# Optimization experiments

Measured on AMD Instinct MI355X. Metric: run time of the kernel, lower is better.

The kernel has to match this reference:

```python
import jax, jax.numpy as jnp
import numpy as np

UNITS = 128
FILTERS = 32
KSIZE = 31
B, T, DV, DQ = 64, 1000, 512, 1024


def setup_inputs() -> dict:
    key = jax.random.key(0)
    ks = jax.random.split(key, 12)
    scale = 0.05
    inp = {
        "query": jax.random.normal(ks[0], (B, DQ), jnp.float32),
        "values": jax.random.normal(ks[1], (B, T, DV), jnp.float32),
        "previous_attention_weights": jax.random.uniform(ks[2], (B, T, 1), jnp.float32),
        # learned params
        "Wq": jax.random.normal(ks[3], (DQ, UNITS), jnp.float32) * scale,
        "bq": jnp.zeros((UNITS,), jnp.float32),
        "Wm": jax.random.normal(ks[4], (DV, UNITS), jnp.float32) * scale,
        "bm": jnp.zeros((UNITS,), jnp.float32),
        "Wv": jax.random.normal(ks[5], (UNITS, 1), jnp.float32) * scale,
        "bv": jnp.zeros((1,), jnp.float32),
        "Wconv": jax.random.normal(ks[6], (KSIZE, 1, FILTERS), jnp.float32) * scale,  # [W, Cin, Cout]
        "Wl": jax.random.normal(ks[7], (FILTERS, UNITS), jnp.float32) * scale,
    }
    return inp


def _forward(query, values, prev_w, Wq, bq, Wm, bm, Wv, bv, Wconv, Wl):
    # location features: Conv1D (same padding, no bias) then Dense(tanh, no bias)
    loc = jax.lax.conv_general_dilated(
        prev_w, Wconv, window_strides=(1,), padding="SAME",
        dimension_numbers=("NWC", "WIO", "NWC"))          # [B, T, FILTERS]
    loc = jnp.tanh(loc @ Wl)                                # [B, T, UNITS]
    q = query @ Wq + bq                                     # [B, UNITS]
    m = values @ Wm + bm                                    # [B, T, UNITS]
    score = jnp.tanh(m + q[:, None, :] + loc) @ Wv + bv     # [B, T, 1]
    attention_weights = jax.nn.softmax(score, axis=1)       # softmax over time
    context = jnp.sum(attention_weights * values, axis=1)   # [B, DV]
    return context, attention_weights


def reference(query, values, previous_attention_weights, Wq, bq, Wm, bm, Wv, bv, Wconv, Wl):
    return _forward(query, values, previous_attention_weights,
                    Wq, bq, Wm, bm, Wv, bv, Wconv, Wl)
```

## Files before the change

### kernel.cpp

```cpp
#include <hip/hip_runtime.h>

#define B_  64
#define T_  1000
#define DV_ 512
#define DQ_ 1024
#define U_  128
#define F_  32
#define KS_ 31
#define P_  16
#define CT_ 63

typedef __attribute__((ext_vector_type(8))) short short8;
typedef __attribute__((ext_vector_type(4))) float f32x4;

__device__ __forceinline__ unsigned pk2(float a, float b) {
    union { float f; unsigned u; } x, y;
    x.f = a; y.f = b;
    unsigned ra = (x.u + 0x7FFFu + ((x.u >> 16) & 1u)) >> 16;
    unsigned rb = (y.u + 0x7FFFu + ((y.u >> 16) & 1u)) >> 16;
    return (ra & 0xFFFFu) | (rb << 16);
}

__device__ __forceinline__ float fast_tanh(float x) {
    return 1.0f - 2.0f / (__expf(2.0f * x) + 1.0f);
}

__device__ __forceinline__ short8 pk8(float4 f0, float4 f1) {
    int4 q;
    q.x = pk2(f0.x, f0.y); q.y = pk2(f0.z, f0.w);
    q.z = pk2(f1.x, f1.y); q.w = pk2(f1.z, f1.w);
    return *(short8*)&q;
}

__global__ __launch_bounds__(1024) void prep_qb_kernel(
    const float* __restrict__ Wm, const float* __restrict__ Wl,
    const float* __restrict__ query, const float* __restrict__ Wq,
    const float* __restrict__ bq, const float* __restrict__ bm,
    short* __restrict__ WmX, short* __restrict__ WlX, float* __restrict__ qb)
{
    __shared__ float sh[DQ_ + 8 * U_];
    int blk = blockIdx.x, tid = threadIdx.x;
    if (blk < 9) {
        int g = blk * 1024 + tid;
        if (g < 8192) {
            int kc = g >> 9, e = g & 511;
            int n = e >> 2, q = e & 3;
            int kb = kc * 32 + q * 8;
            int4 p;
            p.x = pk2(Wm[(kb + 0) * U_ + n], Wm[(kb + 1) * U_ + n]);
            p.y = pk2(Wm[(kb + 2) * U_ + n], Wm[(kb + 3) * U_ + n]);
            p.z = pk2(Wm[(kb + 4) * U_ + n], Wm[(kb + 5) * U_ + n]);
            p.w = pk2(Wm[(kb + 6) * U_ + n], Wm[(kb + 7) * U_ + n]);
            ((int4*)WmX)[g] = p;
        } else if (g < 8704) {
            int e = g - 8192;
            int n = e >> 2, q = e & 3;
            int kb = q * 8;
            int4 p;
            p.x = pk2(Wl[(kb + 0) * U_ + n], Wl[(kb + 1) * U_ + n]);
            p.y = pk2(Wl[(kb + 2) * U_ + n], Wl[(kb + 3) * U_ + n]);
            p.z = pk2(Wl[(kb + 4) * U_ + n], Wl[(kb + 5) * U_ + n]);
            p.w = pk2(Wl[(kb + 6) * U_ + n], Wl[(kb + 7) * U_ + n]);
            ((int4*)WlX)[e] = p;
        }
    } else {
        float* qs = sh;
        float* red = sh + DQ_;
        int b = blk - 9;
        qs[tid] = query[b * DQ_ + tid];
        __syncthreads();
        int u = tid & 127, p = tid >> 7;
        float a = 0.f;
        const float* wp = Wq + (size_t)p * 128 * U_ + u;
        const float* qp = qs + p * 128;
#pragma unroll 8
        for (int k = 0; k < 128; ++k) a += qp[k] * wp[(size_t)k * U_];
        red[p * U_ + u] = a;
        __syncthreads();
        if (tid < U_) {
            float s = bq[tid] + bm[tid];
#pragma unroll
            for (int pp = 0; pp < 8; ++pp) s += red[pp * U_ + tid];
            qb[b * U_ + tid] = s;
        }
    }
}

__global__ __launch_bounds__(256) void score_kernel(
    const float* __restrict__ values, const float* __restrict__ prev,
    const float* __restrict__ Wc, const float* __restrict__ Wv,
    const float* __restrict__ bv, const short* __restrict__ WmX,
    const short* __restrict__ WlX, const float* __restrict__ qb,
    float* __restrict__ scores)
{
    __shared__ float WcS[KS_ * F_];
    __shared__ short AsL[128 * 32];
    __shared__ float qbS[2 * U_];
    __shared__ float WvS[U_];

    const int tid = threadIdx.x;
    const int r0 = blockIdx.x * 128;
    const int b0 = r0 / T_;
    const int b1 = (r0 + 127) / T_;

    for (int i = tid; i < KS_ * F_; i += 256) WcS[i] = Wc[i];
    if (tid < U_) WvS[tid] = Wv[tid];
    {
        int bb = (tid < U_) ? b0 : b1;
        qbS[tid] = qb[bb * U_ + (tid & (U_ - 1))];
    }

    const int wv = tid >> 6, lane = tid & 63;
    const int quad = lane >> 4, m15 = lane & 15;
    const int row0 = wv * 32 + m15;
    const float* aP0 = values + (size_t)(r0 + row0) * DV_ + quad * 8;
    const float* aP1 = aP0 + (size_t)16 * DV_;
    const int4* bW  = (const int4*)WmX + m15 * 4 + quad;
    const int4* blW = (const int4*)WlX + m15 * 4 + quad;

    float4 aq0[2][2], aq1[2][2], aq2[2][2];
    int4 bf0[8], bf1[8];
    aq0[0][0] = *(const float4*)(aP0);      aq0[0][1] = *(const float4*)(aP0 + 4);
    aq0[1][0] = *(const float4*)(aP1);      aq0[1][1] = *(const float4*)(aP1 + 4);
    aq1[0][0] = *(const float4*)(aP0 + 32); aq1[0][1] = *(const float4*)(aP0 + 36);
    aq1[1][0] = *(const float4*)(aP1 + 32); aq1[1][1] = *(const float4*)(aP1 + 36);
#pragma unroll
    for (int c = 0; c < 8; ++c) bf0[c] = bW[c * 64];

    __syncthreads();

#pragma unroll
    for (int it = 0; it < 2; ++it) {
        int idx = tid + it * 256;
        int i = idx & 127, fg = idx >> 7;
        int r = r0 + i;
        int b = r / T_;
        int t = r - b * T_;
        const float* pv = prev + b * T_;
        float a8[8] = {};
#pragma unroll
        for (int k = 0; k < KS_; ++k) {
            int tt = t + k - 15;
            float p = ((unsigned)tt < (unsigned)T_) ? pv[tt] : 0.f;
#pragma unroll
            for (int j = 0; j < 8; ++j) a8[j] += p * WcS[k * F_ + fg * 8 + j];
        }
        int4 pq;
        pq.x = pk2(a8[0], a8[1]); pq.y = pk2(a8[2], a8[3]);
        pq.z = pk2(a8[4], a8[5]); pq.w = pk2(a8[6], a8[7]);
        ((int4*)AsL)[i * 4 + (fg ^ ((i >> 1) & 3))] = pq;
    }
    __syncthreads();

    f32x4 acc[2][8] = {};
    {
        int row1 = row0 + 16;
        short8 afl0 = ((const short8*)AsL)[row0 * 4 + (quad ^ ((row0 >> 1) & 3))];
        short8 afl1 = ((const short8*)AsL)[row1 * 4 + (quad ^ ((row1 >> 1) & 3))];
#pragma unroll
        for (int c = 0; c < 8; ++c) {
            int4 bl = blW[c * 64];
            acc[0][c] = __builtin_amdgcn_mfma_f32_16x16x32_bf16(afl0, *(short8*)&bl, acc[0][c], 0, 0, 0);
            acc[1][c] = __builtin_amdgcn_mfma_f32_16x16x32_bf16(afl1, *(short8*)&bl, acc[1][c], 0, 0, 0);
        }
        int qoff[2][4];
#pragma unroll
        for (int g = 0; g < 2; ++g)
#pragma unroll
            for (int v = 0; v < 4; ++v) {
                int r = r0 + wv * 32 + g * 16 + quad * 4 + v;
                qoff[g][v] = ((r / T_) == b0) ? 0 : U_;
            }
#pragma unroll
        for (int g = 0; g < 2; ++g)
#pragma unroll
            for (int c = 0; c < 8; ++c) {
                int col = c * 16 + m15;
#pragma unroll
                for (int v = 0; v < 4; ++v)
                    acc[g][c][v] = qbS[qoff[g][v] + col] + fast_tanh(acc[g][c][v]);
            }
    }

#pragma unroll
    for (int kc = 0; kc < 16; ++kc) {
        if (kc + 2 < 16) {
            aq2[0][0] = *(const float4*)(aP0 + (kc + 2) * 32);
            aq2[0][1] = *(const float4*)(aP0 + (kc + 2) * 32 + 4);
            aq2[1][0] = *(const float4*)(aP1 + (kc + 2) * 32);
            aq2[1][1] = *(const float4*)(aP1 + (kc + 2) * 32 + 4);
        }
        if (kc + 1 < 16) {
#pragma unroll
            for (int c = 0; c < 8; ++c) bf1[c] = bW[(kc + 1) * 512 + c * 64];
        }
        short8 af0 = pk8(aq0[0][0], aq0[0][1]);
        short8 af1 = pk8(aq0[1][0], aq0[1][1]);
#pragma unroll
        for (int c = 0; c < 8; ++c) {
            acc[0][c] = __builtin_amdgcn_mfma_f32_16x16x32_bf16(af0, *(short8*)&bf0[c], acc[0][c], 0, 0, 0);
            acc[1][c] = __builtin_amdgcn_mfma_f32_16x16x32_bf16(af1, *(short8*)&bf0[c], acc[1][c], 0, 0, 0);
        }
#pragma unroll
        for (int g = 0; g < 2; ++g) {
            aq0[g][0] = aq1[g][0]; aq0[g][1] = aq1[g][1];
            aq1[g][0] = aq2[g][0]; aq1[g][1] = aq2[g][1];
        }
#pragma unroll
        for (int c = 0; c < 8; ++c) bf0[c] = bf1[c];
    }

    float psum[2][4] = {};
#pragma unroll
    for (int g = 0; g < 2; ++g)
#pragma unroll
        for (int c = 0; c < 8; ++c) {
            int col = c * 16 + m15;
            float wvv = WvS[col];
#pragma unroll
            for (int v = 0; v < 4; ++v)
                psum[g][v] += fast_tanh(acc[g][c][v]) * wvv;
        }
#pragma unroll
    for (int off = 1; off < 16; off <<= 1) {
#pragma unroll
        for (int g = 0; g < 2; ++g)
#pragma unroll
            for (int v = 0; v < 4; ++v) psum[g][v] += __shfl_xor(psum[g][v], off);
    }
    if (m15 == 0) {
        float bvv = bv[0];
#pragma unroll
        for (int g = 0; g < 2; ++g)
#pragma unroll
            for (int v = 0; v < 4; ++v)
                scores[r0 + wv * 32 + g * 16 + quad * 4 + v] = psum[g][v] + bvv;
    }
}

__global__ void softmax_kernel(const float* __restrict__ s, float* __restrict__ w) {
    __shared__ float red[4];
    int b = blockIdx.x, tid = threadIdx.x;
    const float* sb = s + b * T_;
    float v[4];
    int tv[4];
#pragma unroll
    for (int i = 0; i < 4; ++i) {
        int t = tid + i * 256;
        tv[i] = t;
        v[i] = (t < T_) ? sb[t] : -1e30f;
    }
    float mx = fmaxf(fmaxf(v[0], v[1]), fmaxf(v[2], v[3]));
#pragma unroll
    for (int off = 32; off >= 1; off >>= 1) mx = fmaxf(mx, __shfl_xor(mx, off));
    int wv = tid >> 6, lane = tid & 63;
    if (lane == 0) red[wv] = mx;
    __syncthreads();
    mx = fmaxf(fmaxf(red[0], red[1]), fmaxf(red[2], red[3]));
    float e[4];
    float sum = 0.f;
#pragma unroll
    for (int i = 0; i < 4; ++i) {
        e[i] = (tv[i] < T_) ? __expf(v[i] - mx) : 0.f;
        sum += e[i];
    }
#pragma unroll
    for (int off = 32; off >= 1; off >>= 1) sum += __shfl_xor(sum, off);
    __syncthreads();
    if (lane == 0) red[wv] = sum;
    __syncthreads();
    sum = red[0] + red[1] + red[2] + red[3];
    float inv = 1.0f / sum;
#pragma unroll
    for (int i = 0; i < 4; ++i)
        if (tv[i] < T_) w[b * T_ + tv[i]] = e[i] * inv;
}

__global__ __launch_bounds__(256) void ctx1_kernel(
    const float* __restrict__ values, const float* __restrict__ w,
    float* __restrict__ part)
{
    __shared__ float wS[CT_];
    __shared__ float4 ps[128];
    int b = blockIdx.x, p = blockIdx.y, tid = threadIdx.x;
    int t0 = p * CT_;
    int len = (T_ - t0 < CT_) ? (T_ - t0) : CT_;
    if (tid < len) wS[tid] = w[b * T_ + t0 + tid];
    __syncthreads();
    int cl = tid & 127, tp = tid >> 7;
    const float* vp = values + ((size_t)b * T_ + t0) * DV_ + cl * 4;
    float4 a = {0.f, 0.f, 0.f, 0.f};
#pragma unroll 4
    for (int t = tp; t < len; t += 2) {
        float4 v = *(const float4*)(vp + (size_t)t * DV_);
        float wt = wS[t];
        a.x += wt * v.x; a.y += wt * v.y; a.z += wt * v.z; a.w += wt * v.w;
    }
    if (tp == 1) ps[cl] = a;
    __syncthreads();
    if (tp == 0) {
        float4 o = ps[cl];
        o.x += a.x; o.y += a.y; o.z += a.z; o.w += a.w;
        *(float4*)(part + ((size_t)(b * P_ + p)) * DV_ + cl * 4) = o;
    }
}

__global__ void ctx2_kernel(const float* __restrict__ part, float* __restrict__ ctx) {
    int b = blockIdx.x, tid = threadIdx.x;
    const float* pp = part + (size_t)b * P_ * DV_ + tid * 4;
    float4 s = {0.f, 0.f, 0.f, 0.f};
#pragma unroll
    for (int p = 0; p < P_; ++p) {
        float4 v = *(const float4*)(pp + (size_t)p * DV_);
        s.x += v.x; s.y += v.y; s.z += v.z; s.w += v.w;
    }
    *(float4*)(ctx + (size_t)b * DV_ + tid * 4) = s;
}

extern "C" void kernel_launch(void* const* d_in, const int* in_sizes, int n_in,
                              void* d_out, int out_size, void* d_ws, size_t ws_size,
                              hipStream_t stream) {
    const float* query  = (const float*)d_in[0];
    const float* values = (const float*)d_in[1];
    const float* prev   = (const float*)d_in[2];
    const float* Wq     = (const float*)d_in[3];
    const float* bq     = (const float*)d_in[4];
    const float* Wm     = (const float*)d_in[5];
    const float* bm     = (const float*)d_in[6];
    const float* Wv     = (const float*)d_in[7];
    const float* bv     = (const float*)d_in[8];
    const float* Wc     = (const float*)d_in[9];
    const float* Wl     = (const float*)d_in[10];

    float* out  = (float*)d_out;
    float* ctx  = out;
    float* attw = out + B_ * DV_;

    char* ws = (char*)d_ws;
    float* qb     = (float*)(ws);
    float* scores = (float*)(ws + 32768);
    short* WmX    = (short*)(ws + 288768);
    short* WlX    = (short*)(ws + 419840);
    float* part   = (float*)(ws + 428032);

    prep_qb_kernel<<<73, 1024, 0, stream>>>(Wm, Wl, query, Wq, bq, bm, WmX, WlX, qb);
    score_kernel<<<500, 256, 0, stream>>>(values, prev, Wc, Wv, bv, WmX, WlX, qb, scores);
    softmax_kernel<<<B_, 256, 0, stream>>>(scores, attw);
    ctx1_kernel<<<dim3(B_, P_), 256, 0, stream>>>(values, attw, part);
    ctx2_kernel<<<B_, 128, 0, stream>>>(part, ctx);
}
```

Before: 273.5 us.

## Halve score tile, split query GEMV across blocks, fuse softmax into context kernel

The score kernel now processes 64 rows per block instead of 128, giving 1000 blocks with one 16-row MFMA group per wave and an occupancy hint of 4 blocks per SIMD, which lowers register pressure. The query projection is split into 16 K-slices computed by 64 blocks, and score blocks sum the partials together with the biases. The separate softmax kernel is removed: each context block recomputes the row max and sum from the scores, then writes its own attention weights. This trades a kernel launch and a write-then-read of the weights for redundant softmax reductions in every (batch, chunk) block.

Measured after the change: 348.3 us. 27.3% more time.

```diff
diff --git a/kernel.cpp b/kernel.cpp
--- a/kernel.cpp
+++ b/kernel.cpp
@@ -32,13 +32,12 @@
     return *(short8*)&q;
 }
 
-__global__ __launch_bounds__(1024) void prep_qb_kernel(
+__global__ __launch_bounds__(1024) void prep_kernel(
     const float* __restrict__ Wm, const float* __restrict__ Wl,
     const float* __restrict__ query, const float* __restrict__ Wq,
-    const float* __restrict__ bq, const float* __restrict__ bm,
-    short* __restrict__ WmX, short* __restrict__ WlX, float* __restrict__ qb)
+    short* __restrict__ WmX, short* __restrict__ WlX, float* __restrict__ partQ)
 {
-    __shared__ float sh[DQ_ + 8 * U_];
+    __shared__ float sh[1024];
     int blk = blockIdx.x, tid = threadIdx.x;
     if (blk < 9) {
         int g = blk * 1024 + tid;
@@ -64,75 +63,74 @@
             ((int4*)WlX)[e] = p;
         }
     } else {
-        float* qs = sh;
-        float* red = sh + DQ_;
-        int b = blk - 9;
-        qs[tid] = query[b * DQ_ + tid];
+        int id = blk - 9;
+        int s  = id >> 2;
+        int bg = id & 3;
+        sh[tid] = query[(size_t)(bg * 16 + (tid >> 6)) * DQ_ + s * 64 + (tid & 63)];
         __syncthreads();
-        int u = tid & 127, p = tid >> 7;
-        float a = 0.f;
-        const float* wp = Wq + (size_t)p * 128 * U_ + u;
-        const float* qp = qs + p * 128;
+        int u = tid & 127, h = tid >> 7;
+        const float* wp = Wq + (size_t)(s * 64) * U_ + u;
+        const float* q0 = sh + (h * 2) * 64;
+        const float* q1 = q0 + 64;
+        float a0 = 0.f, a1 = 0.f;
 #pragma unroll 8
-        for (int k = 0; k < 128; ++k) a += qp[k] * wp[(size_t)k * U_];
-        red[p * U_ + u] = a;
-        __syncthreads();
-        if (tid < U_) {
-            float s = bq[tid] + bm[tid];
-#pragma unroll
-            for (int pp = 0; pp < 8; ++pp) s += red[pp * U_ + tid];
-            qb[b * U_ + tid] = s;
-        }
-    }
-}
-
-__global__ __launch_bounds__(256) void score_kernel(
+        for (int k = 0; k < 64; ++k) {
+            float w = wp[(size_t)k * U_];
+            a0 += q0[k] * w; a1 += q1[k] * w;
+        }
+        int b0i = bg * 16 + h * 2;
+        partQ[s * 8192 + b0i * 128 + u]       = a0;
+        partQ[s * 8192 + (b0i + 1) * 128 + u] = a1;
+    }
+}
+
+__global__ __launch_bounds__(256, 4) void score_kernel(
     const float* __restrict__ values, const float* __restrict__ prev,
     const float* __restrict__ Wc, const float* __restrict__ Wv,
     const float* __restrict__ bv, const short* __restrict__ WmX,
-    const short* __restrict__ WlX, const float* __restrict__ qb,
+    const short* __restrict__ WlX, const float* __restrict__ partQ,
+    const float* __restrict__ bq, const float* __restrict__ bm,
     float* __restrict__ scores)
 {
     __shared__ float WcS[KS_ * F_];
-    __shared__ short AsL[128 * 32];
+    __shared__ short AsL[64 * 32];
     __shared__ float qbS[2 * U_];
     __shared__ float WvS[U_];
 
     const int tid = threadIdx.x;
-    const int r0 = blockIdx.x * 128;
+    const int r0 = blockIdx.x * 64;
     const int b0 = r0 / T_;
-    const int b1 = (r0 + 127) / T_;
+    const int b1 = (r0 + 63) / T_;
 
     for (int i = tid; i < KS_ * F_; i += 256) WcS[i] = Wc[i];
     if (tid < U_) WvS[tid] = Wv[tid];
     {
+        int u = tid & (U_ - 1);
         int bb = (tid < U_) ? b0 : b1;
-        qbS[tid] = qb[bb * U_ + (tid & (U_ - 1))];
+        float s = bq[u] + bm[u];
+#pragma unroll
+        for (int sl = 0; sl < 16; ++sl) s += partQ[sl * 8192 + bb * 128 + u];
+        qbS[tid] = s;
     }
 
     const int wv = tid >> 6, lane = tid & 63;
     const int quad = lane >> 4, m15 = lane & 15;
-    const int row0 = wv * 32 + m15;
-    const float* aP0 = values + (size_t)(r0 + row0) * DV_ + quad * 8;
-    const float* aP1 = aP0 + (size_t)16 * DV_;
+    const int row0 = wv * 16 + m15;
+    const float* aP = values + (size_t)(r0 + row0) * DV_ + quad * 8;
     const int4* bW  = (const int4*)WmX + m15 * 4 + quad;
     const int4* blW = (const int4*)WlX + m15 * 4 + quad;
 
-    float4 aq0[2][2], aq1[2][2], aq2[2][2];
-    int4 bf0[8], bf1[8];
-    aq0[0][0] = *(const float4*)(aP0);      aq0[0][1] = *(const float4*)(aP0 + 4);
-    aq0[1][0] = *(const float4*)(aP1);      aq0[1][1] = *(const float4*)(aP1 + 4);
-    aq1[0][0] = *(const float4*)(aP0 + 32); aq1[0][1] = *(const float4*)(aP0 + 36);
-    aq1[1][0] = *(const float4*)(aP1 + 32); aq1[1][1] = *(const float4*)(aP1 + 36);
-#pragma unroll
-    for (int c = 0; c < 8; ++c) bf0[c] = bW[c * 64];
-
-    __syncthreads();
-
-#pragma unroll
-    for (int it = 0; it < 2; ++it) {
-        int idx = tid + it * 256;
-        int i = idx & 127, fg = idx >> 7;
+    float4 aq0[2], aq1[2], aq2[2];
+    int4 bf[8];
+    aq0[0] = *(const float4*)(aP);      aq0[1] = *(const float4*)(aP + 4);
+    aq1[0] = *(const float4*)(aP + 32); aq1[1] = *(const float4*)(aP + 36);
+#pragma unroll
+    for (int c = 0; c < 8; ++c) bf[c] = bW[c * 64];
+
+    __syncthreads();
+
+    {
+        int i = tid & 63, fg = tid >> 6;
         int r = r0 + i;
         int b = r / T_;
         int t = r - b * T_;
@@ -152,96 +150,77 @@
     }
     __syncthreads();
 
-    f32x4 acc[2][8] = {};
+    f32x4 acc[8] = {};
     {
-        int row1 = row0 + 16;
-        short8 afl0 = ((const short8*)AsL)[row0 * 4 + (quad ^ ((row0 >> 1) & 3))];
-        short8 afl1 = ((const short8*)AsL)[row1 * 4 + (quad ^ ((row1 >> 1) & 3))];
+        short8 afl = ((const short8*)AsL)[row0 * 4 + (quad ^ ((row0 >> 1) & 3))];
 #pragma unroll
         for (int c = 0; c < 8; ++c) {
             int4 bl = blW[c * 64];
-            acc[0][c] = __builtin_amdgcn_mfma_f32_16x16x32_bf16(afl0, *(short8*)&bl, acc[0][c], 0, 0, 0);
-            acc[1][c] = __builtin_amdgcn_mfma_f32_16x16x32_bf16(afl1, *(short8*)&bl, acc[1][c], 0, 0, 0);
-        }
-        int qoff[2][4];
-#pragma unroll
-        for (int g = 0; g < 2; ++g)
-#pragma unroll
-            for (int v = 0; v < 4; ++v) {
-                int r = r0 + wv * 32 + g * 16 + quad * 4 + v;
-                qoff[g][v] = ((r / T_) == b0) ? 0 : U_;
-            }
-#pragma unroll
-        for (int g = 0; g < 2; ++g)
-#pragma unroll
-            for (int c = 0; c < 8; ++c) {
-                int col = c * 16 + m15;
-#pragma unroll
-                for (int v = 0; v < 4; ++v)
-                    acc[g][c][v] = qbS[qoff[g][v] + col] + fast_tanh(acc[g][c][v]);
-            }
+            acc[c] = __builtin_amdgcn_mfma_f32_16x16x32_bf16(afl, *(short8*)&bl, acc[c], 0, 0, 0);
+        }
+        int qoff[4];
+#pragma unroll
+        for (int v = 0; v < 4; ++v) {
+            int r = r0 + wv * 16 + quad * 4 + v;
+            qoff[v] = ((r / T_) == b0) ? 0 : U_;
+        }
+#pragma unroll
+        for (int c = 0; c < 8; ++c) {
+            int col = c * 16 + m15;
+#pragma unroll
+            for (int v = 0; v < 4; ++v)
+                acc[c][v] = qbS[qoff[v] + col] + fast_tanh(acc[c][v]);
+        }
     }
 
 #pragma unroll
     for (int kc = 0; kc < 16; ++kc) {
         if (kc + 2 < 16) {
-            aq2[0][0] = *(const float4*)(aP0 + (kc + 2) * 32);
-            aq2[0][1] = *(const float4*)(aP0 + (kc + 2) * 32 + 4);
-            aq2[1][0] = *(const float4*)(aP1 + (kc + 2) * 32);
-            aq2[1][1] = *(const float4*)(aP1 + (kc + 2) * 32 + 4);
-        }
-        if (kc + 1 < 16) {
-#pragma unroll
-            for (int c = 0; c < 8; ++c) bf1[c] = bW[(kc + 1) * 512 + c * 64];
-        }
-        short8 af0 = pk8(aq0[0][0], aq0[0][1]);
-        short8 af1 = pk8(aq0[1][0], aq0[1][1]);
+            aq2[0] = *(const float4*)(aP + (kc + 2) * 32);
+            aq2[1] = *(const float4*)(aP + (kc + 2) * 32 + 4);
+        }
+        short8 af = pk8(aq0[0], aq0[1]);
 #pragma unroll
         for (int c = 0; c < 8; ++c) {
-            acc[0][c] = __builtin_amdgcn_mfma_f32_16x16x32_bf16(af0, *(short8*)&bf0[c], acc[0][c], 0, 0, 0);
-            acc[1][c] = __builtin_amdgcn_mfma_f32_16x16x32_bf16(af1, *(short8*)&bf0[c], acc[1][c], 0, 0, 0);
-        }
-#pragma unroll
-        for (int g = 0; g < 2; ++g) {
-            aq0[g][0] = aq1[g][0]; aq0[g][1] = aq1[g][1];
-            aq1[g][0] = aq2[g][0]; aq1[g][1] = aq2[g][1];
-        }
-#pragma unroll
-        for (int c = 0; c < 8; ++c) bf0[c] = bf1[c];
-    }
-
-    float psum[2][4] = {};
-#pragma unroll
-    for (int g = 0; g < 2; ++g)
-#pragma unroll
-        for (int c = 0; c < 8; ++c) {
-            int col = c * 16 + m15;
-            float wvv = WvS[col];
-#pragma unroll
-            for (int v = 0; v < 4; ++v)
-                psum[g][v] += fast_tanh(acc[g][c][v]) * wvv;
-        }
+            acc[c] = __builtin_amdgcn_mfma_f32_16x16x32_bf16(af, *(short8*)&bf[c], acc[c], 0, 0, 0);
+            if (kc + 1 < 16) bf[c] = bW[(kc + 1) * 512 + c * 64];
+        }
+        aq0[0] = aq1[0]; aq0[1] = aq1[1];
+        aq1[0] = aq2[0]; aq1[1] = aq2[1];
+    }
+
+    float psum[4] = {};
+#pragma unroll
+    for (int c = 0; c < 8; ++c) {
+        int col = c * 16 + m15;
+        float wvv = WvS[col];
+#pragma unroll
+        for (int v = 0; v < 4; ++v)
+            psum[v] += fast_tanh(acc[c][v]) * wvv;
+    }
 #pragma unroll
     for (int off = 1; off < 16; off <<= 1) {
 #pragma unroll
-        for (int g = 0; g < 2; ++g)
-#pragma unroll
-            for (int v = 0; v < 4; ++v) psum[g][v] += __shfl_xor(psum[g][v], off);
+        for (int v = 0; v < 4; ++v) psum[v] += __shfl_xor(psum[v], off);
     }
     if (m15 == 0) {
         float bvv = bv[0];
 #pragma unroll
-        for (int g = 0; g < 2; ++g)
-#pragma unroll
-            for (int v = 0; v < 4; ++v)
-                scores[r0 + wv * 32 + g * 16 + quad * 4 + v] = psum[g][v] + bvv;
-    }
-}
-
-__global__ void softmax_kernel(const float* __restrict__ s, float* __restrict__ w) {
+        for (int v = 0; v < 4; ++v)
+            scores[r0 + wv * 16 + quad * 4 + v] = psum[v] + bvv;
+    }
+}
+
+__global__ __launch_bounds__(256) void ctx1_kernel(
+    const float* __restrict__ values, const float* __restrict__ scores,
+    float* __restrict__ attw, float* __restrict__ part)
+{
+    __shared__ float wS[CT_];
+    __shared__ float4 ps[128];
     __shared__ float red[4];
-    int b = blockIdx.x, tid = threadIdx.x;
-    const float* sb = s + b * T_;
+    int b = blockIdx.x, p = blockIdx.y, tid = threadIdx.x;
+    const float* sb = scores + b * T_;
+
     float v[4];
     int tv[4];
 #pragma unroll
@@ -253,48 +232,38 @@
     float mx = fmaxf(fmaxf(v[0], v[1]), fmaxf(v[2], v[3]));
 #pragma unroll
     for (int off = 32; off >= 1; off >>= 1) mx = fmaxf(mx, __shfl_xor(mx, off));
-    int wv = tid >> 6, lane = tid & 63;
-    if (lane == 0) red[wv] = mx;
+    int wvi = tid >> 6, lane = tid & 63;
+    if (lane == 0) red[wvi] = mx;
     __syncthreads();
     mx = fmaxf(fmaxf(red[0], red[1]), fmaxf(red[2], red[3]));
-    float e[4];
     float sum = 0.f;
 #pragma unroll
-    for (int i = 0; i < 4; ++i) {
-        e[i] = (tv[i] < T_) ? __expf(v[i] - mx) : 0.f;
-        sum += e[i];
-    }
+    for (int i = 0; i < 4; ++i)
+        sum += (tv[i] < T_) ? __expf(v[i] - mx) : 0.f;
 #pragma unroll
     for (int off = 32; off >= 1; off >>= 1) sum += __shfl_xor(sum, off);
     __syncthreads();
-    if (lane == 0) red[wv] = sum;
-    __syncthreads();
-    sum = red[0] + red[1] + red[2] + red[3];
-    float inv = 1.0f / sum;
-#pragma unroll
-    for (int i = 0; i < 4; ++i)
-        if (tv[i] < T_) w[b * T_ + tv[i]] = e[i] * inv;
-}
-
-__global__ __launch_bounds__(256) void ctx1_kernel(
-    const float* __restrict__ values, const float* __restrict__ w,
-    float* __restrict__ part)
-{
-    __shared__ float wS[CT_];
-    __shared__ float4 ps[128];
-    int b = blockIdx.x, p = blockIdx.y, tid = threadIdx.x;
+    if (lane == 0) red[wvi] = sum;
+    __syncthreads();
+    float inv = 1.0f / (red[0] + red[1] + red[2] + red[3]);
+
     int t0 = p * CT_;
     int len = (T_ - t0 < CT_) ? (T_ - t0) : CT_;
-    if (tid < len) wS[tid] = w[b * T_ + t0 + tid];
-    __syncthreads();
+    if (tid < len) {
+        float e = __expf(sb[t0 + tid] - mx) * inv;
+        wS[tid] = e;
+        attw[b * T_ + t0 + tid] = e;
+    }
+    __syncthreads();
+
     int cl = tid & 127, tp = tid >> 7;
     const float* vp = values + ((size_t)b * T_ + t0) * DV_ + cl * 4;
     float4 a = {0.f, 0.f, 0.f, 0.f};
 #pragma unroll 4
     for (int t = tp; t < len; t += 2) {
-        float4 v = *(const float4*)(vp + (size_t)t * DV_);
+        float4 vv = *(const float4*)(vp + (size_t)t * DV_);
         float wt = wS[t];
-        a.x += wt * v.x; a.y += wt * v.y; a.z += wt * v.z; a.w += wt * v.w;
+        a.x += wt * vv.x; a.y += wt * vv.y; a.z += wt * vv.z; a.w += wt * vv.w;
     }
     if (tp == 1) ps[cl] = a;
     __syncthreads();
@@ -337,15 +306,15 @@
     float* attw = out + B_ * DV_;
 
     char* ws = (char*)d_ws;
-    float* qb     = (float*)(ws);
-    float* scores = (float*)(ws + 32768);
-    short* WmX    = (short*)(ws + 288768);
-    short* WlX    = (short*)(ws + 419840);
-    float* part   = (float*)(ws + 428032);
-
-    prep_qb_kernel<<<73, 1024, 0, stream>>>(Wm, Wl, query, Wq, bq, bm, WmX, WlX, qb);
-    score_kernel<<<500, 256, 0, stream>>>(values, prev, Wc, Wv, bv, WmX, WlX, qb, scores);
-    softmax_kernel<<<B_, 256, 0, stream>>>(scores, attw);
-    ctx1_kernel<<<dim3(B_, P_), 256, 0, stream>>>(values, attw, part);
+    float* part   = (float*)(ws);
+    float* partQ  = (float*)(ws);
+    float* scores = (float*)(ws + 2097152);
+    short* WmX    = (short*)(ws + 2097152 + 262144);
+    short* WlX    = (short*)(ws + 2097152 + 262144 + 131072);
+
+    prep_kernel<<<73, 1024, 0, stream>>>(Wm, Wl, query, Wq, WmX, WlX, partQ);
+    score_kernel<<<1000, 256, 0, stream>>>(values, prev, Wc, Wv, bv, WmX, WlX,
+                                           partQ, bq, bm, scores);
+    ctx1_kernel<<<dim3(B_, P_), 256, 0, stream>>>(values, scores, attw, part);
     ctx2_kernel<<<B_, 128, 0, stream>>>(part, ctx);
 }
```
